# Optimization experiments

Measured on AMD Instinct MI355X. Metric: run time of the kernel, lower is better.

The kernel has to match this reference:

```python
import math
import jax, jax.numpy as jnp
import numpy as np

B, S, H = 8, 2048, 1024
NH = 1
DH = H // NH          # head dim == hidden since NH=1 (required by module's math)
DT = 64               # distance_type


def setup_inputs() -> dict:
    key = jax.random.key(0)
    ks = jax.random.split(key, 10)
    hidden_states = jax.random.normal(ks[0], (B, S, H), dtype=jnp.float32)
    attention_mask = jnp.zeros((B, 1, 1, S), dtype=jnp.float32)
    word_word_relation = jax.random.randint(ks[1], (B, S, S), 0, DT, dtype=jnp.int32)
    init = 0.02
    Wq = jax.random.normal(ks[2], (H, H), dtype=jnp.float32) * init
    bq = jnp.zeros((H,), dtype=jnp.float32)
    Wk = jax.random.normal(ks[3], (H, H), dtype=jnp.float32) * init
    bk = jnp.zeros((H,), dtype=jnp.float32)
    Wv = jax.random.normal(ks[4], (H, H), dtype=jnp.float32) * init
    bv = jnp.zeros((H,), dtype=jnp.float32)
    dist_emb = jax.random.normal(ks[5], (DT, H), dtype=jnp.float32) * init
    dist_emb = dist_emb.at[0].set(0.0)  # padding_idx=0
    return {
        "hidden_states": hidden_states,
        "attention_mask": attention_mask,
        "word_word_relation": word_word_relation,
        "Wq": Wq, "bq": bq, "Wk": Wk, "bk": bk, "Wv": Wv, "bv": bv,
        "dist_emb": dist_emb,
    }


def reference(hidden_states, attention_mask, word_word_relation,
              Wq, bq, Wk, bk, Wv, bv, dist_emb):
    b, s, h = hidden_states.shape
    def heads(x):  # [b,s,h] -> [b,nh,s,dh]
        return x.reshape(b, s, NH, DH).transpose(0, 2, 1, 3)
    q = heads(hidden_states @ Wq.T + bq)
    k = heads(hidden_states @ Wk.T + bk)
    v = heads(hidden_states @ Wv.T + bv)

    scores = jnp.einsum('bhqd,bhkd->bhqk', q, k)                 # [b,nh,s,s]
    word_dot_distance = jnp.einsum('bhqd,td->bhqt', q, dist_emb) # [b,nh,s,DT]

    idx = word_word_relation[:, None, :, :]                      # [b,1,s,s]
    bias = jnp.take_along_axis(word_dot_distance, idx, axis=3)
    mask_out = (word_word_relation == 1)[:, None].astype(scores.dtype)
    bias = bias * mask_out

    scores = (scores + bias) / math.sqrt(DH) + attention_mask
    probs = jax.nn.softmax(scores, axis=-1)
    ctx = jnp.einsum('bhqk,bhkd->bhqd', probs, v)
    ctx = ctx.transpose(0, 2, 1, 3).reshape(b, s, h)
    return ctx
```

## Files before the change

### kernel.cpp

```cpp
#include <hip/hip_runtime.h>

typedef unsigned short u16;
typedef __bf16 bf16x8 __attribute__((ext_vector_type(8)));
typedef u16 u16x8 __attribute__((ext_vector_type(8)));
typedef float f32x4 __attribute__((ext_vector_type(4)));

#define S_LEN 2048
#define H_LEN 1024

__device__ __forceinline__ u16 f2b(float f) {
  unsigned u = __float_as_uint(f);
  return (u16)((u + 0x7FFFu + ((u >> 16) & 1u)) >> 16);
}
__device__ __forceinline__ float b2f(u16 h) { return __uint_as_float(((unsigned)h) << 16); }

#define GLOAD16(gp, lp)                                   \
  __builtin_amdgcn_global_load_lds(                       \
      (__attribute__((address_space(1))) void*)(gp),      \
      (__attribute__((address_space(3))) void*)(lp), 16, 0, 0)

__global__ __launch_bounds__(256) void prep_kernel(
    const float* __restrict__ X, const float* __restrict__ Wq,
    const float* __restrict__ Wk, const float* __restrict__ Wv,
    const float* __restrict__ bq, const float* __restrict__ bk,
    const float* __restrict__ bv, const float* __restrict__ dist,
    u16* __restrict__ Xbf, u16* __restrict__ Wbf, float* __restrict__ b_all,
    u16* __restrict__ de1, float* __restrict__ lsum, float* __restrict__ d1) {
  size_t tid = (size_t)blockIdx.x * blockDim.x + threadIdx.x;
  size_t nth = (size_t)gridDim.x * blockDim.x;
  for (size_t i = tid; i < 4194304u; i += nth) {
    float4 v = ((const float4*)X)[i];
    ushort4 o; o.x = f2b(v.x); o.y = f2b(v.y); o.z = f2b(v.z); o.w = f2b(v.w);
    ((ushort4*)Xbf)[i] = o;
  }
  for (size_t i = tid; i < 786432u; i += nth) {
    int which = (int)(i >> 18);
    size_t off = i & 262143u;
    const float4* src = (const float4*)(which == 0 ? Wq : (which == 1 ? Wk : Wv));
    float4 v = src[off];
    ushort4 o; o.x = f2b(v.x); o.y = f2b(v.y); o.z = f2b(v.z); o.w = f2b(v.w);
    ((ushort4*)Wbf)[i] = o;
  }
  for (size_t i = tid; i < 256u; i += nth) {
    float4 v = ((const float4*)(dist + H_LEN))[i];
    ushort4 o; o.x = f2b(v.x); o.y = f2b(v.y); o.z = f2b(v.z); o.w = f2b(v.w);
    ((ushort4*)de1)[i] = o;
  }
  for (size_t i = tid; i < 3072u; i += nth)
    b_all[i] = (i < 1024) ? bq[i] : (i < 2048 ? bk[i - 1024] : bv[i - 2048]);
  for (size_t i = tid; i < 16384u; i += nth) { lsum[i] = 0.f; d1[i] = 0.f; }
}

__global__ __launch_bounds__(256) void relprep_kernel(const int* __restrict__ rel,
                                                      unsigned* __restrict__ bits) {
  size_t tid = (size_t)blockIdx.x * blockDim.x + threadIdx.x;
  size_t nth = (size_t)gridDim.x * blockDim.x;
  const int4* r4 = (const int4*)rel;
  for (size_t wi = tid; wi < 1048576u; wi += nth) {
    const int4* s = r4 + wi * 8;
    unsigned m = 0;
#pragma unroll
    for (int u = 0; u < 8; ++u) {
      int4 v = s[u];
      m |= (unsigned)(v.x == 1) << (u * 4 + 0);
      m |= (unsigned)(v.y == 1) << (u * 4 + 1);
      m |= (unsigned)(v.z == 1) << (u * 4 + 2);
      m |= (unsigned)(v.w == 1) << (u * 4 + 3);
    }
    bits[wi] = m;
  }
}

struct GArgs {
  const u16* A; const u16* B;
  long long sA, sB;
  int ldA, ldB, K;
  u16 *Qo, *Ko, *Vo; const float* b_all; const u16* de1; float* d1;
  const unsigned* relbits; const float* mask; u16* P; float* lsum;
  const float* lin; float* outp;
};

template <int EPI>
__global__ __launch_bounds__(256) void gemm_nt(GArgs g) {
  const int bz = blockIdx.z;
  int bx = blockIdx.x, by = blockIdx.y;
  if constexpr (EPI == 0) {
    const int lin = by * 24 + bx;
    const int band = lin / (24 * 8), rem = lin % (24 * 8);
    by = band * 8 + (rem & 7);
    bx = rem >> 3;
  }
  const u16* Abase = g.A + (size_t)bz * g.sA;
  const u16* Bbase = g.B + (size_t)bz * g.sB;
  const int m0 = by * 128, n0 = bx * 128;

  __shared__ u16 smem[16384];
  u16* As = smem;
  u16* Bs = smem + 8192;

  const int tid = threadIdx.x;
  const int lane = tid & 63, w = tid >> 6;
  const int wm = w >> 1, wn = w & 1;
  const int l15 = lane & 15, quad = lane >> 4;

  f32x4 acc[4][4];
  const f32x4 zero = {0.f, 0.f, 0.f, 0.f};
#pragma unroll
  for (int a = 0; a < 4; ++a)
#pragma unroll
    for (int b = 0; b < 4; ++b) acc[a][b] = zero;

  const int c0 = tid, c1 = tid + 256;
  const u16* ga0 = Abase + (size_t)(m0 + (c0 >> 2)) * g.ldA + (c0 & 3) * 8;
  const u16* ga1 = Abase + (size_t)(m0 + (c1 >> 2)) * g.ldA + (c1 & 3) * 8;
  const u16* gb0 = Bbase + (size_t)(n0 + (c0 >> 2)) * g.ldB + (c0 & 3) * 8;
  const u16* gb1 = Bbase + (size_t)(n0 + (c1 >> 2)) * g.ldB + (c1 & 3) * 8;
  u16* la0 = As + c0 * 8; u16* la1 = As + c1 * 8;
  u16* lb0 = Bs + c0 * 8; u16* lb1 = Bs + c1 * 8;

  for (int kt = 0; kt < g.K; kt += 64) {
    __syncthreads();
    GLOAD16(ga0 + kt, la0);      GLOAD16(ga0 + kt + 32, la0 + 4096);
    GLOAD16(ga1 + kt, la1);      GLOAD16(ga1 + kt + 32, la1 + 4096);
    GLOAD16(gb0 + kt, lb0);      GLOAD16(gb0 + kt + 32, lb0 + 4096);
    GLOAD16(gb1 + kt, lb1);      GLOAD16(gb1 + kt + 32, lb1 + 4096);
    __syncthreads();
#pragma unroll
    for (int s = 0; s < 2; ++s) {
      bf16x8 af[4], bfb[4];
#pragma unroll
      for (int t = 0; t < 4; ++t) {
        af[t]  = *(const bf16x8*)&As[s * 4096 + (wm * 64 + t * 16 + l15) * 32 + quad * 8];
        bfb[t] = *(const bf16x8*)&Bs[s * 4096 + (wn * 64 + t * 16 + l15) * 32 + quad * 8];
      }
#pragma unroll
      for (int mt = 0; mt < 4; ++mt)
#pragma unroll
        for (int nt = 0; nt < 4; ++nt)
          acc[mt][nt] = __builtin_amdgcn_mfma_f32_16x16x32_bf16(af[mt], bfb[nt], acc[mt][nt], 0, 0, 0);
    }
  }
  __syncthreads();

  const int nbase = n0 + wn * 64;

  if constexpr (EPI == 0) {
    const int which = n0 >> 10;
    float bv4[4], dw[4];
#pragma unroll
    for (int nt = 0; nt < 4; ++nt) {
      bv4[nt] = g.b_all[nbase + nt * 16 + l15];
      dw[nt] = (which == 0) ? b2f(g.de1[nbase + nt * 16 + l15]) : 0.f;
    }
#pragma unroll
    for (int mt = 0; mt < 4; ++mt)
#pragma unroll
      for (int r = 0; r < 4; ++r) {
        const int row = wm * 64 + mt * 16 + quad * 4 + r;
        float part = 0.f;
#pragma unroll
        for (int nt = 0; nt < 4; ++nt) {
          const float v = acc[mt][nt][r] + bv4[nt];
          part += v * dw[nt];
          const int col = wn * 64 + nt * 16 + l15;
          const int chunkS = (col >> 3) ^ (row & 15);
          smem[row * 128 + chunkS * 8 + (col & 7)] = f2b(v);
        }
        if (which == 0) {
          part += __shfl_xor(part, 1);
          part += __shfl_xor(part, 2);
          part += __shfl_xor(part, 4);
          part += __shfl_xor(part, 8);
          if (l15 == 0) atomicAdd(&g.d1[m0 + row], part);
        }
      }
    __syncthreads();
    u16* dstbuf = which == 0 ? g.Qo : (which == 1 ? g.Ko : g.Vo);
    const int nl0 = n0 & 1023;
#pragma unroll
    for (int p = 0; p < 8; ++p) {
      const int flat = p * 256 + tid;
      const int row = flat >> 4, chunk = flat & 15;
      const int chunkS = chunk ^ (row & 15);
      u16x8 v = *(const u16x8*)&smem[row * 128 + chunkS * 8];
      *(u16x8*)(dstbuf + (size_t)(m0 + row) * H_LEN + nl0 + chunk * 8) = v;
    }
  }

  if constexpr (EPI == 1) {
    float mk[4];
#pragma unroll
    for (int nt = 0; nt < 4; ++nt) mk[nt] = g.mask[bz * S_LEN + nbase + nt * 16 + l15];
    const size_t bSS = (size_t)bz * S_LEN * S_LEN;
#pragma unroll
    for (int mt = 0; mt < 4; ++mt)
#pragma unroll
      for (int r = 0; r < 4; ++r) {
        const int row = wm * 64 + mt * 16 + quad * 4 + r;
        const int gi = bz * S_LEN + m0 + row;
        const float d1v = g.d1[gi] * 0.03125f;
        const unsigned w0 = g.relbits[(size_t)gi * 64 + (nbase >> 5)];
        const unsigned w1 = g.relbits[(size_t)gi * 64 + (nbase >> 5) + 1];
        float psum = 0.f;
#pragma unroll
        for (int nt = 0; nt < 4; ++nt) {
          const unsigned word = (nt & 2) ? w1 : w0;
          const int pos = (nt * 16 + l15) & 31;
          const float bias = ((word >> pos) & 1) ? d1v : 0.f;
          const float logit = acc[mt][nt][r] * 0.03125f + bias + mk[nt];
          const float pv = __expf(logit);
          psum += pv;
          const int col = wn * 64 + nt * 16 + l15;
          const int chunkS = (col >> 3) ^ (row & 15);
          smem[row * 128 + chunkS * 8 + (col & 7)] = f2b(pv);
        }
        psum += __shfl_xor(psum, 1);
        psum += __shfl_xor(psum, 2);
        psum += __shfl_xor(psum, 4);
        psum += __shfl_xor(psum, 8);
        if (l15 == 0) atomicAdd(&g.lsum[gi], psum);
      }
    __syncthreads();
#pragma unroll
    for (int p = 0; p < 8; ++p) {
      const int flat = p * 256 + tid;
      const int row = flat >> 4, chunk = flat & 15;
      const int chunkS = chunk ^ (row & 15);
      u16x8 v = *(const u16x8*)&smem[row * 128 + chunkS * 8];
      *(u16x8*)(g.P + bSS + (size_t)(m0 + row) * S_LEN + n0 + chunk * 8) = v;
    }
  }

  if constexpr (EPI == 2) {
    const size_t ob = (size_t)bz * S_LEN * H_LEN;
#pragma unroll
    for (int mt = 0; mt < 4; ++mt)
#pragma unroll
      for (int r = 0; r < 4; ++r) {
        const int i = m0 + wm * 64 + mt * 16 + quad * 4 + r;
        const float inv = 1.0f / g.lin[bz * S_LEN + i];
        const size_t rowo = ob + (size_t)i * H_LEN;
#pragma unroll
        for (int nt = 0; nt < 4; ++nt) {
          const int d = n0 + wn * 64 + nt * 16 + l15;
          g.outp[rowo + d] = acc[mt][nt][r] * inv;
        }
      }
  }
}

__global__ __launch_bounds__(256) void transpose_v(const u16* __restrict__ V,
                                                   u16* __restrict__ Vt) {
  const int b = blockIdx.z;
  const int j0 = blockIdx.x * 64;
  const int d0 = blockIdx.y * 64;
  __shared__ u16 t[64][72];
  const int tid = threadIdx.x;
  const int tr = tid >> 4;
  const int tc = (tid & 15) * 4;
#pragma unroll
  for (int p = 0; p < 4; ++p) {
    const int jl = p * 16 + tr;
    const u16* src = V + ((size_t)b * S_LEN + (j0 + jl)) * H_LEN + d0 + tc;
    ushort4 v = *(const ushort4*)src;
    t[jl][tc + 0] = v.x; t[jl][tc + 1] = v.y; t[jl][tc + 2] = v.z; t[jl][tc + 3] = v.w;
  }
  __syncthreads();
#pragma unroll
  for (int p = 0; p < 4; ++p) {
    const int dl = p * 16 + tr;
    ushort4 v;
    v.x = t[tc + 0][dl]; v.y = t[tc + 1][dl]; v.z = t[tc + 2][dl]; v.w = t[tc + 3][dl];
    *(ushort4*)(Vt + ((size_t)b * H_LEN + (d0 + dl)) * S_LEN + j0 + tc) = v;
  }
}

extern "C" void kernel_launch(void* const* d_in, const int* in_sizes, int n_in,
                              void* d_out, int out_size, void* d_ws, size_t ws_size,
                              hipStream_t stream) {
  (void)in_sizes; (void)n_in; (void)out_size; (void)ws_size;
  const float* X    = (const float*)d_in[0];
  const float* mask = (const float*)d_in[1];
  const int*   rel  = (const int*)d_in[2];
  const float* Wq   = (const float*)d_in[3];
  const float* bq   = (const float*)d_in[4];
  const float* Wk   = (const float*)d_in[5];
  const float* bk   = (const float*)d_in[6];
  const float* Wv   = (const float*)d_in[7];
  const float* bv   = (const float*)d_in[8];
  const float* dist = (const float*)d_in[9];
  float* out = (float*)d_out;

  char* p = (char*)d_ws;
  u16* Xbf = (u16*)p;      p += (size_t)16384 * 1024 * 2;
  u16* Wbf = (u16*)p;      p += (size_t)3072 * 1024 * 2;
  float* b_all = (float*)p; p += 3072 * 4;
  u16* de1 = (u16*)p;      p += 4096;
  u16* Qb = (u16*)p;       p += (size_t)16384 * 1024 * 2;
  u16* Kb = (u16*)p;       p += (size_t)16384 * 1024 * 2;
  u16* Vb = (u16*)p;       p += (size_t)16384 * 1024 * 2;
  u16* Vt = (u16*)p;       p += (size_t)16384 * 1024 * 2;
  float* d1 = (float*)p;   p += 16384 * 4;
  float* lsum = (float*)p; p += 16384 * 4;
  u16* P = (u16*)p;        p += (size_t)8 * 2048 * 2048 * 2;
  unsigned* relbits = (unsigned*)Xbf;

  prep_kernel<<<1024, 256, 0, stream>>>(X, Wq, Wk, Wv, bq, bk, bv, dist,
                                        Xbf, Wbf, b_all, de1, lsum, d1);

  GArgs g0 = {};
  g0.A = Xbf; g0.B = Wbf; g0.sA = 0; g0.sB = 0;
  g0.ldA = 1024; g0.ldB = 1024; g0.K = 1024;
  g0.Qo = Qb; g0.Ko = Kb; g0.Vo = Vb; g0.b_all = b_all; g0.de1 = de1; g0.d1 = d1;
  gemm_nt<0><<<dim3(24, 128, 1), dim3(256, 1, 1), 0, stream>>>(g0);

  relprep_kernel<<<1024, 256, 0, stream>>>(rel, relbits);
  transpose_v<<<dim3(32, 16, 8), dim3(256, 1, 1), 0, stream>>>(Vb, Vt);

  GArgs g1 = {};
  g1.A = Qb; g1.B = Kb; g1.sA = 2048LL * 1024; g1.sB = 2048LL * 1024;
  g1.ldA = 1024; g1.ldB = 1024; g1.K = 1024;
  g1.relbits = relbits; g1.d1 = d1; g1.mask = mask; g1.P = P; g1.lsum = lsum;
  gemm_nt<1><<<dim3(16, 16, 8), dim3(256, 1, 1), 0, stream>>>(g1);

  GArgs g2 = {};
  g2.A = P; g2.B = Vt; g2.sA = 2048LL * 2048; g2.sB = 1024LL * 2048;
  g2.ldA = 2048; g2.ldB = 2048; g2.K = 2048;
  g2.lin = lsum; g2.outp = out;
  gemm_nt<2><<<dim3(8, 16, 8), dim3(256, 1, 1), 0, stream>>>(g2);
}
```

Measured before the change: 684.1 us.

## Compute softmax row sums via MFMA with ones in PV GEMM; merge relprep

```diff
diff --git a/kernel.cpp b/kernel.cpp
--- a/kernel.cpp
+++ b/kernel.cpp
@@ -24,8 +24,9 @@
     const float* __restrict__ Wk, const float* __restrict__ Wv,
     const float* __restrict__ bq, const float* __restrict__ bk,
     const float* __restrict__ bv, const float* __restrict__ dist,
+    const int* __restrict__ rel,
     u16* __restrict__ Xbf, u16* __restrict__ Wbf, float* __restrict__ b_all,
-    u16* __restrict__ de1, float* __restrict__ lsum, float* __restrict__ d1) {
+    u16* __restrict__ de1, unsigned* __restrict__ bits, float* __restrict__ d1) {
   size_t tid = (size_t)blockIdx.x * blockDim.x + threadIdx.x;
   size_t nth = (size_t)gridDim.x * blockDim.x;
   for (size_t i = tid; i < 4194304u; i += nth) {
@@ -41,20 +42,6 @@
     ushort4 o; o.x = f2b(v.x); o.y = f2b(v.y); o.z = f2b(v.z); o.w = f2b(v.w);
     ((ushort4*)Wbf)[i] = o;
   }
-  for (size_t i = tid; i < 256u; i += nth) {
-    float4 v = ((const float4*)(dist + H_LEN))[i];
-    ushort4 o; o.x = f2b(v.x); o.y = f2b(v.y); o.z = f2b(v.z); o.w = f2b(v.w);
-    ((ushort4*)de1)[i] = o;
-  }
-  for (size_t i = tid; i < 3072u; i += nth)
-    b_all[i] = (i < 1024) ? bq[i] : (i < 2048 ? bk[i - 1024] : bv[i - 2048]);
-  for (size_t i = tid; i < 16384u; i += nth) { lsum[i] = 0.f; d1[i] = 0.f; }
-}
-
-__global__ __launch_bounds__(256) void relprep_kernel(const int* __restrict__ rel,
-                                                      unsigned* __restrict__ bits) {
-  size_t tid = (size_t)blockIdx.x * blockDim.x + threadIdx.x;
-  size_t nth = (size_t)gridDim.x * blockDim.x;
   const int4* r4 = (const int4*)rel;
   for (size_t wi = tid; wi < 1048576u; wi += nth) {
     const int4* s = r4 + wi * 8;
@@ -69,6 +56,14 @@
     }
     bits[wi] = m;
   }
+  for (size_t i = tid; i < 256u; i += nth) {
+    float4 v = ((const float4*)(dist + H_LEN))[i];
+    ushort4 o; o.x = f2b(v.x); o.y = f2b(v.y); o.z = f2b(v.z); o.w = f2b(v.w);
+    ((ushort4*)de1)[i] = o;
+  }
+  for (size_t i = tid; i < 3072u; i += nth)
+    b_all[i] = (i < 1024) ? bq[i] : (i < 2048 ? bk[i - 1024] : bv[i - 2048]);
+  for (size_t i = tid; i < 16384u; i += nth) d1[i] = 0.f;
 }
 
 struct GArgs {
@@ -76,8 +71,8 @@
   long long sA, sB;
   int ldA, ldB, K;
   u16 *Qo, *Ko, *Vo; const float* b_all; const u16* de1; float* d1;
-  const unsigned* relbits; const float* mask; u16* P; float* lsum;
-  const float* lin; float* outp;
+  const unsigned* relbits; const float* mask; u16* P;
+  float* outp;
 };
 
 template <int EPI>
@@ -104,11 +99,17 @@
   const int l15 = lane & 15, quad = lane >> 4;
 
   f32x4 acc[4][4];
+  f32x4 acc_sum[4];
   const f32x4 zero = {0.f, 0.f, 0.f, 0.f};
 #pragma unroll
-  for (int a = 0; a < 4; ++a)
+  for (int a = 0; a < 4; ++a) {
+    acc_sum[a] = zero;
 #pragma unroll
     for (int b = 0; b < 4; ++b) acc[a][b] = zero;
+  }
+  bf16x8 ones;
+#pragma unroll
+  for (int i = 0; i < 8; ++i) ones[i] = (__bf16)1.0f;
 
   const int c0 = tid, c1 = tid + 256;
   const u16* ga0 = Abase + (size_t)(m0 + (c0 >> 2)) * g.ldA + (c0 & 3) * 8;
@@ -134,10 +135,13 @@
         bfb[t] = *(const bf16x8*)&Bs[s * 4096 + (wn * 64 + t * 16 + l15) * 32 + quad * 8];
       }
 #pragma unroll
-      for (int mt = 0; mt < 4; ++mt)
+      for (int mt = 0; mt < 4; ++mt) {
 #pragma unroll
         for (int nt = 0; nt < 4; ++nt)
           acc[mt][nt] = __builtin_amdgcn_mfma_f32_16x16x32_bf16(af[mt], bfb[nt], acc[mt][nt], 0, 0, 0);
+        if constexpr (EPI == 2)
+          acc_sum[mt] = __builtin_amdgcn_mfma_f32_16x16x32_bf16(af[mt], ones, acc_sum[mt], 0, 0, 0);
+      }
     }
   }
   __syncthreads();
@@ -201,7 +205,6 @@
         const float d1v = g.d1[gi] * 0.03125f;
         const unsigned w0 = g.relbits[(size_t)gi * 64 + (nbase >> 5)];
         const unsigned w1 = g.relbits[(size_t)gi * 64 + (nbase >> 5) + 1];
-        float psum = 0.f;
 #pragma unroll
         for (int nt = 0; nt < 4; ++nt) {
           const unsigned word = (nt & 2) ? w1 : w0;
@@ -209,16 +212,10 @@
           const float bias = ((word >> pos) & 1) ? d1v : 0.f;
           const float logit = acc[mt][nt][r] * 0.03125f + bias + mk[nt];
           const float pv = __expf(logit);
-          psum += pv;
           const int col = wn * 64 + nt * 16 + l15;
           const int chunkS = (col >> 3) ^ (row & 15);
           smem[row * 128 + chunkS * 8 + (col & 7)] = f2b(pv);
         }
-        psum += __shfl_xor(psum, 1);
-        psum += __shfl_xor(psum, 2);
-        psum += __shfl_xor(psum, 4);
-        psum += __shfl_xor(psum, 8);
-        if (l15 == 0) atomicAdd(&g.lsum[gi], psum);
       }
     __syncthreads();
 #pragma unroll
@@ -238,7 +235,7 @@
 #pragma unroll
       for (int r = 0; r < 4; ++r) {
         const int i = m0 + wm * 64 + mt * 16 + quad * 4 + r;
-        const float inv = 1.0f / g.lin[bz * S_LEN + i];
+        const float inv = 1.0f / acc_sum[mt][r];
         const size_t rowo = ob + (size_t)i * H_LEN;
 #pragma unroll
         for (int nt = 0; nt < 4; ++nt) {
@@ -301,12 +298,11 @@
   u16* Vb = (u16*)p;       p += (size_t)16384 * 1024 * 2;
   u16* Vt = (u16*)p;       p += (size_t)16384 * 1024 * 2;
   float* d1 = (float*)p;   p += 16384 * 4;
-  float* lsum = (float*)p; p += 16384 * 4;
+  unsigned* relbits = (unsigned*)p; p += (size_t)1048576 * 4;
   u16* P = (u16*)p;        p += (size_t)8 * 2048 * 2048 * 2;
-  unsigned* relbits = (unsigned*)Xbf;
-
-  prep_kernel<<<1024, 256, 0, stream>>>(X, Wq, Wk, Wv, bq, bk, bv, dist,
-                                        Xbf, Wbf, b_all, de1, lsum, d1);
+
+  prep_kernel<<<1024, 256, 0, stream>>>(X, Wq, Wk, Wv, bq, bk, bv, dist, rel,
+                                        Xbf, Wbf, b_all, de1, relbits, d1);
 
   GArgs g0 = {};
   g0.A = Xbf; g0.B = Wbf; g0.sA = 0; g0.sB = 0;
@@ -314,18 +310,17 @@
   g0.Qo = Qb; g0.Ko = Kb; g0.Vo = Vb; g0.b_all = b_all; g0.de1 = de1; g0.d1 = d1;
   gemm_nt<0><<<dim3(24, 128, 1), dim3(256, 1, 1), 0, stream>>>(g0);
 
-  relprep_kernel<<<1024, 256, 0, stream>>>(rel, relbits);
   transpose_v<<<dim3(32, 16, 8), dim3(256, 1, 1), 0, stream>>>(Vb, Vt);
 
   GArgs g1 = {};
   g1.A = Qb; g1.B = Kb; g1.sA = 2048LL * 1024; g1.sB = 2048LL * 1024;
   g1.ldA = 1024; g1.ldB = 1024; g1.K = 1024;
-  g1.relbits = relbits; g1.d1 = d1; g1.mask = mask; g1.P = P; g1.lsum = lsum;
+  g1.relbits = relbits; g1.d1 = d1; g1.mask = mask; g1.P = P;
   gemm_nt<1><<<dim3(16, 16, 8), dim3(256, 1, 1), 0, stream>>>(g1);
 
   GArgs g2 = {};
   g2.A = P; g2.B = Vt; g2.sA = 2048LL * 2048; g2.sB = 1024LL * 2048;
   g2.ldA = 2048; g2.ldB = 2048; g2.K = 2048;
-  g2.lin = lsum; g2.outp = out;
+  g2.outp = out;
   gemm_nt<2><<<dim3(8, 16, 8), dim3(256, 1, 1), 0, stream>>>(g2);
 }
```

Result: faster. 631.1 us (-7.7%).
